# Kernel optimization log

Hardware: AMD Instinct MI355X
Metric: run time of the kernel (lower is better)

## Reference

```python
import jax, jax.numpy as jnp
import numpy as np

K = 3; PAD = 1; STRIDE = 1; EPS = 1e-5


def setup_inputs() -> dict:
    key = jax.random.key(0)
    k0, k1, k2 = jax.random.split(key, 3)
    B, C, H, W, O = 4, 256, 64, 64, 256
    x = jax.random.normal(k0, (B, C, H, W), jnp.float32)
    # offset conv: small random weights so offsets are nontrivial but bounded
    w_off = jax.random.normal(k1, (2 * K * K, C, K, K), jnp.float32) * 0.01
    b_off = jnp.zeros((2 * K * K,), jnp.float32)
    # kaiming normal, mode=fan_out: std = sqrt(2 / (O*K*K))
    w_def = jax.random.normal(k2, (O, C, K, K), jnp.float32) * np.float32(np.sqrt(2.0 / (O * K * K)))
    gamma = jnp.ones((O,), jnp.float32)
    beta = jnp.zeros((O,), jnp.float32)
    return {"x": x, "w_off": w_off, "b_off": b_off, "w_def": w_def, "gamma": gamma, "beta": beta}


def _bilinear_gather(x, py, px):
    """x: [B,C,H,W]; py,px: [B,K2,Ho,Wo] float sample coords.
    Returns [B,K2,Ho,Wo,C] with zero padding outside (per-corner masking,
    matching torchvision deform_conv2d)."""
    B, C, H, W = x.shape
    y0f = jnp.floor(py); x0f = jnp.floor(px)
    wy1 = py - y0f; wy0 = 1.0 - wy1
    wx1 = px - x0f; wx0 = 1.0 - wx1
    bidx = jnp.arange(B)[:, None, None, None]

    def corner(yf, xf, wgt):
        valid = (yf >= 0) & (yf <= H - 1) & (xf >= 0) & (xf <= W - 1)
        yc = jnp.clip(yf.astype(jnp.int32), 0, H - 1)
        xc = jnp.clip(xf.astype(jnp.int32), 0, W - 1)
        v = x[bidx, :, yc, xc]  # [B,K2,Ho,Wo,C] (advanced idx moves C last)
        return v * (wgt * valid)[..., None]

    return (corner(y0f, x0f, wy0 * wx0) + corner(y0f, x0f + 1.0, wy0 * wx1)
            + corner(y0f + 1.0, x0f, wy1 * wx0) + corner(y0f + 1.0, x0f + 1.0, wy1 * wx1))


def _forward(x, w_off, b_off, w_def, gamma, beta):
    B, C, H, W = x.shape
    O = w_def.shape[0]
    K2 = K * K
    # 1) offset-predicting conv
    off = jax.lax.conv_general_dilated(x, w_off, (STRIDE, STRIDE), ((PAD, PAD), (PAD, PAD)))
    off = off + b_off[None, :, None, None]
    Ho, Wo = off.shape[2], off.shape[3]
    off = off.reshape(B, K2, 2, Ho, Wo)  # pairs (dy, dx) per kernel tap
    # 2) deformable sampling locations
    ky, kx = jnp.meshgrid(jnp.arange(K, dtype=jnp.float32), jnp.arange(K, dtype=jnp.float32), indexing='ij')
    base_y = (jnp.arange(Ho, dtype=jnp.float32) * STRIDE - PAD)
    base_x = (jnp.arange(Wo, dtype=jnp.float32) * STRIDE - PAD)
    py = off[:, :, 0] + ky.reshape(K2)[None, :, None, None] + base_y[None, None, :, None]
    px = off[:, :, 1] + kx.reshape(K2)[None, :, None, None] + base_x[None, None, None, :]
    vals = _bilinear_gather(x, py, px)  # [B,K2,Ho,Wo,C]
    # 3) deform conv GEMM (bias=False)
    out = jnp.einsum('bkhwc,ock->bohw', vals, w_def.reshape(O, C, K2))
    # 4) BatchNorm (training mode: batch stats) + ReLU
    mean = out.mean(axis=(0, 2, 3))
    var = out.var(axis=(0, 2, 3))
    out = (out - mean[None, :, None, None]) * (gamma * jax.lax.rsqrt(var + EPS))[None, :, None, None]
    out = out + beta[None, :, None, None]
    return jax.nn.relu(out)


def reference(x, w_off, b_off, w_def, gamma, beta):
    return _forward(x, w_off, b_off, w_def, gamma, beta)
```

## Files before the change

kernel.cpp:

```cpp
#include <hip/hip_runtime.h>
#include <hip/hip_bf16.h>

typedef unsigned int  uint;
typedef unsigned short ushort;
typedef short bf16x8 __attribute__((ext_vector_type(8)));
typedef float f32x4  __attribute__((ext_vector_type(4)));

#define HW   4096
#define KD   2304

__device__ __forceinline__ void load_lds16(const void* g, void* l) {
    __builtin_amdgcn_global_load_lds((const __attribute__((address_space(1))) void*)g,
                                     (__attribute__((address_space(3))) void*)l, 16, 0, 0);
}
__device__ __forceinline__ float blo(uint u) { return __uint_as_float(u << 16); }
__device__ __forceinline__ float bhi(uint u) { return __uint_as_float(u & 0xffff0000u); }
__device__ __forceinline__ uint pack2(float e, float o) {
    __hip_bfloat16 he = __float2bfloat16(e), ho = __float2bfloat16(o);
    return (uint)(*(ushort*)&he) | ((uint)(*(ushort*)&ho) << 16);
}

__global__ void prep_x2(const float* __restrict__ x, uint* __restrict__ x2) {
    int idx = blockIdx.x * 256 + threadIdx.x;
    int a  = idx & 4095;
    int cp = (idx >> 12) & 127;
    int b  = idx >> 19;
    const float* p = x + ((size_t)(b * 256 + 2 * cp)) * HW + a;
    x2[idx] = pack2(p[0], p[HW]);
}

__global__ void prep_bt(const float* __restrict__ w_def, ushort* __restrict__ bt) {
    int idx = blockIdx.x * 256 + threadIdx.x;
    int c   = idx & 255;
    int tap = (idx >> 8) % 9;
    int o   = idx / KD;
    __hip_bfloat16 h = __float2bfloat16(w_def[(o * 256 + c) * 9 + tap]);
    bt[idx] = *(ushort*)&h;
}

__global__ void prep_bt0(const float* __restrict__ w_off, ushort* __restrict__ bt0) {
    int idx = blockIdx.x * 256 + threadIdx.x;
    int c   = idx & 255;
    int tap = (idx >> 8) % 9;
    int j   = idx / KD;
    float v = (j < 18) ? w_off[(j * 256 + c) * 9 + tap] : 0.f;
    __hip_bfloat16 h = __float2bfloat16(v);
    bt0[idx] = *(ushort*)&h;
}

__global__ __launch_bounds__(512) void gemm_off(const uint* __restrict__ x2,
                                                const ushort* __restrict__ bt0,
                                                const float* __restrict__ b_off,
                                                float* __restrict__ off) {
    int id = blockIdx.x;
    int xcd = id & 7;
    int b = xcd >> 1, h = (xcd & 1) * 32 + (id >> 3);
    int t = threadIdx.x, wv = t >> 6, lane = t & 63;
    int mrow = lane & 15, quad = lane >> 4;
    int mq = wv & 3, nn = wv >> 2;

    __shared__ uint   lX[3 * 32 * 64];
    __shared__ ushort lB[32 * 576];

    f32x4 acc = {0.f, 0.f, 0.f, 0.f};

    for (int cb = 0; cb < 4; ++cb) {
#pragma unroll
        for (int s = 0; s < 3; ++s) {
            int q  = s * 8 + wv;
            int dy = q >> 3;
            int y  = h + dy - 1;
            int dl = (q & 7) * 256 + lane * 4;
            int cp = dl >> 6, w4 = dl & 63;
            uint* dst = &lX[q * 256 + lane * 4];
            if ((unsigned)y < 64u) {
                const uint* src = x2 + ((size_t)(b * 128 + cb * 32 + cp)) * HW + y * 64 + w4;
                load_lds16(src, &lX[q * 256]);
            } else {
                uint4 z = {0u, 0u, 0u, 0u};
                *(uint4*)dst = z;
            }
        }
#pragma unroll
        for (int s = 0; s < 5; ++s) {
            int q = s * 8 + wv;
            if (q < 36) {
                int e = q * 512 + lane * 8;
                int o  = e / 576;
                int r  = e - o * 576;
                int chp = r >> 3;
                int ch  = chp ^ (o & 7);
                int tap = ch >> 3, k8 = ch & 7;
                const ushort* src = bt0 + (size_t)o * KD + tap * 256 + cb * 64 + k8 * 8;
                load_lds16(src, &lB[q * 512]);
            }
        }
        __syncthreads();

#pragma unroll
        for (int tap = 0; tap < 9; ++tap) {
            int dy = tap / 3, dx = tap % 3;
            int xx = mq * 16 + mrow + dx - 1;
            bool vx = (unsigned)xx < 64u;
#pragma unroll
            for (int kb = 0; kb < 2; ++kb) {
                int cp0 = kb * 16 + quad * 4;
                uint ad[4];
#pragma unroll
                for (int i = 0; i < 4; ++i)
                    ad[i] = vx ? lX[(dy * 32 + cp0 + i) * 64 + xx] : 0u;
                bf16x8 af = *(bf16x8*)ad;
                int o = nn * 16 + mrow;
                int chs = (tap * 8 + (((kb * 4 + quad)) ^ (o & 7)));
                bf16x8 bfr = *(const bf16x8*)&lB[o * 576 + chs * 8];
                acc = __builtin_amdgcn_mfma_f32_16x16x32_bf16(af, bfr, acc, 0, 0, 0);
            }
        }
        __syncthreads();
    }
    {
        int o = nn * 16 + mrow;
        float bias = (o < 18) ? b_off[o] : 0.f;
        f32x4 v = acc;
        v.x += bias; v.y += bias; v.z += bias; v.w += bias;
        int wpos = mq * 16 + quad * 4;
        *(f32x4*)(off + ((size_t)(b * 32 + o)) * HW + h * 64 + wpos) = v;
    }
}

__global__ __launch_bounds__(1024, 4) void fused_main(const uint* __restrict__ x2,
                                                      const ushort* __restrict__ bt,
                                                      const float* __restrict__ off,
                                                      float* __restrict__ out,
                                                      float* __restrict__ stats) {
    int id = blockIdx.x;
    int xcd = id & 7;
    int b = xcd >> 1, h = (xcd & 1) * 32 + (id >> 3);
    int t = threadIdx.x;
    int wv = t >> 6, lane = t & 63;
    int mrow = lane & 15, quad = lane >> 4;
    bool producer = (wv < 8);
    int w  = t & 63;
    int cq = (t >> 6) & 7;

    __shared__ int    sAc[4][9][64];
    __shared__ float  sWc[4][9][64];
    __shared__ ushort lA[2][64 * 64];
    __shared__ ushort lB[2][256 * 64];

    for (int i = t; i < 576; i += 1024) {
        int tap = i >> 6, ww = i & 63;
        int hw = h * 64 + ww;
        float oy = off[((size_t)(b * 32 + 2 * tap)) * HW + hw];
        float ox = off[((size_t)(b * 32 + 2 * tap + 1)) * HW + hw];
        float py = oy + (float)(tap / 3 + h - 1);
        float px = ox + (float)(tap % 3 + ww - 1);
        float y0f = floorf(py), x0f = floorf(px);
        float wy1 = py - y0f, wx1 = px - x0f;
        float wy0 = 1.f - wy1, wx0 = 1.f - wx1;
        bool vy0 = (y0f >= 0.f) && (y0f <= 63.f);
        bool vy1 = (y0f >= -1.f) && (y0f <= 62.f);
        bool vx0 = (x0f >= 0.f) && (x0f <= 63.f);
        bool vx1 = (x0f >= -1.f) && (x0f <= 62.f);
        int iy0 = min(max((int)y0f, 0), 63),  iy1 = min(max((int)y0f + 1, 0), 63);
        int ix0 = min(max((int)x0f, 0), 63),  ix1 = min(max((int)x0f + 1, 0), 63);
        sAc[0][tap][ww] = iy0 * 64 + ix0;
        sAc[1][tap][ww] = iy0 * 64 + ix1;
        sAc[2][tap][ww] = iy1 * 64 + ix0;
        sAc[3][tap][ww] = iy1 * 64 + ix1;
        sWc[0][tap][ww] = wy0 * wx0 * (float)(vy0 && vx0);
        sWc[1][tap][ww] = wy0 * wx1 * (float)(vy0 && vx1);
        sWc[2][tap][ww] = wy1 * wx0 * (float)(vy1 && vx0);
        sWc[3][tap][ww] = wy1 * wx1 * (float)(vy1 && vx1);
    }
    __syncthreads();

    f32x4 acc[4][2];
#pragma unroll
    for (int m = 0; m < 4; ++m)
#pragma unroll
        for (int n = 0; n < 2; ++n) acc[m][n] = {0.f, 0.f, 0.f, 0.f};

    const uint* xb = x2 + (size_t)(b * 128) * HW;

    auto stage = [&](int sl, ushort* lAb, ushort* lBb) {
        int tap = sl >> 2, cb = sl & 3;
        int a0 = sAc[0][tap][w], a1 = sAc[1][tap][w], a2 = sAc[2][tap][w], a3 = sAc[3][tap][w];
        float f0 = sWc[0][tap][w], f1 = sWc[1][tap][w], f2 = sWc[2][tap][w], f3 = sWc[3][tap][w];
        const uint* xp = xb + (size_t)(cb * 32 + cq * 4) * HW;
        uint u0[4], u1[4], u2[4], u3[4];
#pragma unroll
        for (int j = 0; j < 4; ++j) {
            const uint* pq = xp + (size_t)j * HW;
            u0[j] = pq[a0]; u1[j] = pq[a1]; u2[j] = pq[a2]; u3[j] = pq[a3];
        }
#pragma unroll
        for (int s2 = 0; s2 < 4; ++s2) {
            int e = s2 * 512 + t;
            int o = e >> 3, pp = e & 7;
            int k8 = pp ^ (o & 7);
            const ushort* src = bt + (size_t)o * KD + tap * 256 + cb * 64 + k8 * 8;
            load_lds16(src, &lBb[(e & ~63) * 8]);
        }
        uint r[4];
#pragma unroll
        for (int j = 0; j < 4; ++j) {
            float ev = f0 * blo(u0[j]) + f1 * blo(u1[j]) + f2 * blo(u2[j]) + f3 * blo(u3[j]);
            float ov = f0 * bhi(u0[j]) + f1 * bhi(u1[j]) + f2 * bhi(u2[j]) + f3 * bhi(u3[j]);
            r[j] = pack2(ev, ov);
        }
        uint4 g = {r[0], r[1], r[2], r[3]};
        *(uint4*)&lAb[w * 64 + ((cq ^ (w & 7)) * 8)] = g;
    };

    if (producer) stage(0, lA[0], lB[0]);

    int p = 0;
    for (int s = 0; s < 36; ++s) {
        __syncthreads();
        if (producer) {
            if (s + 1 < 36) stage(s + 1, lA[p ^ 1], lB[p ^ 1]);
        } else {
            int wvc = wv - 8;
#pragma unroll
            for (int kb = 0; kb < 2; ++kb) {
                bf16x8 af[4];
#pragma unroll
                for (int m = 0; m < 4; ++m) {
                    int r = m * 16 + mrow;
                    af[m] = *(const bf16x8*)&lA[p][r * 64 + (((kb * 4 + quad) ^ (r & 7)) * 8)];
                }
#pragma unroll
                for (int n = 0; n < 2; ++n) {
                    int r = wvc * 32 + n * 16 + mrow;
                    bf16x8 bfr = *(const bf16x8*)&lB[p][r * 64 + (((kb * 4 + quad) ^ (r & 7)) * 8)];
#pragma unroll
                    for (int m = 0; m < 4; ++m)
                        acc[m][n] = __builtin_amdgcn_mfma_f32_16x16x32_bf16(af[m], bfr, acc[m][n], 0, 0, 0);
                }
            }
        }
        p ^= 1;
    }

    if (!producer) {
        int wvc = wv - 8;
#pragma unroll
        for (int n = 0; n < 2; ++n) {
            int o = wvc * 32 + n * 16 + mrow;
            float ss = 0.f, qq = 0.f;
#pragma unroll
            for (int m = 0; m < 4; ++m) {
                int pos = m * 16 + quad * 4;
                f32x4 v = acc[m][n];
                *(f32x4*)(out + ((size_t)(b * 256 + o)) * HW + h * 64 + pos) = v;
                ss += v.x + v.y + v.z + v.w;
                qq += v.x * v.x + v.y * v.y + v.z * v.z + v.w * v.w;
            }
            ss += __shfl_xor(ss, 16); ss += __shfl_xor(ss, 32);
            qq += __shfl_xor(qq, 16); qq += __shfl_xor(qq, 32);
            if (quad == 0) {
                atomicAdd(&stats[o], ss);
                atomicAdd(&stats[512 + o], qq);
            }
        }
    }
}

__global__ void bn_finalize(const float* __restrict__ stats,
                            const float* __restrict__ gamma,
                            float* __restrict__ ms) {
    int o = threadIdx.x;
    float S = stats[o], S2 = stats[512 + o];
    float m  = S / 16384.f;
    float var = S2 / 16384.f - m * m;
    ms[o]       = m;
    ms[256 + o] = gamma[o] * rsqrtf(var + 1e-5f);
}

__global__ void bn_apply(float* __restrict__ out,
                         const float* __restrict__ ms,
                         const float* __restrict__ beta) {
    int idx4 = blockIdx.x * 256 + threadIdx.x;
    int o = (idx4 >> 10) & 255;
    float4 v = ((const float4*)out)[idx4];
    float mu = ms[o], sc = ms[256 + o], be = beta[o];
    v.x = fmaxf((v.x - mu) * sc + be, 0.f);
    v.y = fmaxf((v.y - mu) * sc + be, 0.f);
    v.z = fmaxf((v.z - mu) * sc + be, 0.f);
    v.w = fmaxf((v.w - mu) * sc + be, 0.f);
    ((float4*)out)[idx4] = v;
}

extern "C" void kernel_launch(void* const* d_in, const int* in_sizes, int n_in,
                              void* d_out, int out_size, void* d_ws, size_t ws_size,
                              hipStream_t stream) {
    const float* x     = (const float*)d_in[0];
    const float* w_off = (const float*)d_in[1];
    const float* b_off = (const float*)d_in[2];
    const float* w_def = (const float*)d_in[3];
    const float* gamma = (const float*)d_in[4];
    const float* beta  = (const float*)d_in[5];
    float* out = (float*)d_out;

    char* ws = (char*)d_ws;
    uint*   x2    = (uint*)ws;
    ushort* bt    = (ushort*)(ws + 8388608);
    ushort* bt0   = (ushort*)(ws + 9568256);
    float*  off   = (float*)(ws + 9715712);
    float*  stats = (float*)(ws + 11812864);
    float*  ms    = (float*)(ws + 11816960);

    hipMemsetAsync(stats, 0, 4096, stream);
    prep_x2 <<<8192, 256, 0, stream>>>(x, x2);
    prep_bt <<<2304, 256, 0, stream>>>(w_def, bt);
    prep_bt0<<<288,  256, 0, stream>>>(w_off, bt0);
    gemm_off<<<256, 512, 0, stream>>>(x2, bt0, b_off, off);
    fused_main<<<256, 1024, 0, stream>>>(x2, bt, off, out, stats);
    bn_finalize<<<1, 256, 0, stream>>>(stats, gamma, ms);
    bn_apply<<<4096, 256, 0, stream>>>(out, ms, beta);
}
```

Baseline: 179.9 us.

## Store bf16 input channel-innermost (NHWC) for vectorized deformable gathers

The packed bf16 copy of x is now written in a pixel-major, channel-innermost layout through an LDS transpose in the prep kernel. The deformable sampling stage can then fetch four channel pairs per corner with one 16-byte load instead of four scattered 4-byte loads. The offset conv's LDS tile is reorganised to match, with an XOR swizzle so its A fragments become single 16-byte LDS reads. The cost is a more involved transpose in prep and new swizzled indexing that must stay correct.

```diff
diff --git a/kernel.cpp b/kernel.cpp
--- a/kernel.cpp
+++ b/kernel.cpp
@@ -20,13 +20,27 @@
     return (uint)(*(ushort*)&he) | ((uint)(*(ushort*)&ho) << 16);
 }
 
-__global__ void prep_x2(const float* __restrict__ x, uint* __restrict__ x2) {
-    int idx = blockIdx.x * 256 + threadIdx.x;
-    int a  = idx & 4095;
-    int cp = (idx >> 12) & 127;
-    int b  = idx >> 19;
-    const float* p = x + ((size_t)(b * 256 + 2 * cp)) * HW + a;
-    x2[idx] = pack2(p[0], p[HW]);
+__global__ void prep_x2t(const float* __restrict__ x, uint* __restrict__ x2t) {
+    __shared__ uint tl[32][65];
+    int bidx = blockIdx.x;
+    int ab  = bidx & 63;
+    int cpb = (bidx >> 6) & 3;
+    int b   = bidx >> 8;
+    int t = threadIdx.x;
+#pragma unroll
+    for (int i = 0; i < 8; ++i) {
+        int idx = i * 256 + t;
+        int cp = idx >> 6, a = idx & 63;
+        const float* p = x + ((size_t)(b * 256 + (cpb * 32 + cp) * 2)) * HW + ab * 64 + a;
+        tl[cp][a] = pack2(p[0], p[HW]);
+    }
+    __syncthreads();
+#pragma unroll
+    for (int i = 0; i < 8; ++i) {
+        int idx = i * 256 + t;
+        int a = idx >> 5, cp = idx & 31;
+        x2t[((size_t)b * 4096 + ab * 64 + a) * 128 + cpb * 32 + cp] = tl[cp][a];
+    }
 }
 
 __global__ void prep_bt(const float* __restrict__ w_def, ushort* __restrict__ bt) {
@@ -48,7 +62,7 @@
     bt0[idx] = *(ushort*)&h;
 }
 
-__global__ __launch_bounds__(512) void gemm_off(const uint* __restrict__ x2,
+__global__ __launch_bounds__(512) void gemm_off(const uint* __restrict__ x2t,
                                                 const ushort* __restrict__ bt0,
                                                 const float* __restrict__ b_off,
                                                 float* __restrict__ off) {
@@ -59,7 +73,7 @@
     int mrow = lane & 15, quad = lane >> 4;
     int mq = wv & 3, nn = wv >> 2;
 
-    __shared__ uint   lX[3 * 32 * 64];
+    __shared__ uint   lX[3 * 64 * 32];
     __shared__ ushort lB[32 * 576];
 
     f32x4 acc = {0.f, 0.f, 0.f, 0.f};
@@ -67,18 +81,18 @@
     for (int cb = 0; cb < 4; ++cb) {
 #pragma unroll
         for (int s = 0; s < 3; ++s) {
-            int q  = s * 8 + wv;
-            int dy = q >> 3;
-            int y  = h + dy - 1;
-            int dl = (q & 7) * 256 + lane * 4;
-            int cp = dl >> 6, w4 = dl & 63;
-            uint* dst = &lX[q * 256 + lane * 4];
+            int q   = s * 8 + wv;
+            int dy  = q >> 3;
+            int y   = h + dy - 1;
+            int sub = q & 7;
+            int wl  = sub * 8 + (lane >> 3);
+            int cps = ((lane & 7) ^ ((lane >> 3) & 7)) * 4;
             if ((unsigned)y < 64u) {
-                const uint* src = x2 + ((size_t)(b * 128 + cb * 32 + cp)) * HW + y * 64 + w4;
+                const uint* src = x2t + ((size_t)(b * 4096 + y * 64 + wl)) * 128 + cb * 32 + cps;
                 load_lds16(src, &lX[q * 256]);
             } else {
                 uint4 z = {0u, 0u, 0u, 0u};
-                *(uint4*)dst = z;
+                *(uint4*)&lX[q * 256 + lane * 4] = z;
             }
         }
 #pragma unroll
@@ -102,14 +116,13 @@
             int dy = tap / 3, dx = tap % 3;
             int xx = mq * 16 + mrow + dx - 1;
             bool vx = (unsigned)xx < 64u;
+            int xc = min(max(xx, 0), 63);
 #pragma unroll
             for (int kb = 0; kb < 2; ++kb) {
                 int cp0 = kb * 16 + quad * 4;
-                uint ad[4];
-#pragma unroll
-                for (int i = 0; i < 4; ++i)
-                    ad[i] = vx ? lX[(dy * 32 + cp0 + i) * 64 + xx] : 0u;
-                bf16x8 af = *(bf16x8*)ad;
+                uint4 ad = {0u, 0u, 0u, 0u};
+                if (vx) ad = *(const uint4*)&lX[dy * 2048 + xc * 32 + (cp0 ^ ((xc & 7) * 4))];
+                bf16x8 af = *(bf16x8*)&ad;
                 int o = nn * 16 + mrow;
                 int chs = (tap * 8 + (((kb * 4 + quad)) ^ (o & 7)));
                 bf16x8 bfr = *(const bf16x8*)&lB[o * 576 + chs * 8];
@@ -128,7 +141,7 @@
     }
 }
 
-__global__ __launch_bounds__(1024, 4) void fused_main(const uint* __restrict__ x2,
+__global__ __launch_bounds__(1024, 4) void fused_main(const uint* __restrict__ x2t,
                                                       const ushort* __restrict__ bt,
                                                       const float* __restrict__ off,
                                                       float* __restrict__ out,
@@ -181,19 +194,17 @@
 #pragma unroll
         for (int n = 0; n < 2; ++n) acc[m][n] = {0.f, 0.f, 0.f, 0.f};
 
-    const uint* xb = x2 + (size_t)(b * 128) * HW;
+    const uint* xb = x2t + (size_t)b * 4096 * 128;
 
     auto stage = [&](int sl, ushort* lAb, ushort* lBb) {
         int tap = sl >> 2, cb = sl & 3;
         int a0 = sAc[0][tap][w], a1 = sAc[1][tap][w], a2 = sAc[2][tap][w], a3 = sAc[3][tap][w];
         float f0 = sWc[0][tap][w], f1 = sWc[1][tap][w], f2 = sWc[2][tap][w], f3 = sWc[3][tap][w];
-        const uint* xp = xb + (size_t)(cb * 32 + cq * 4) * HW;
-        uint u0[4], u1[4], u2[4], u3[4];
-#pragma unroll
-        for (int j = 0; j < 4; ++j) {
-            const uint* pq = xp + (size_t)j * HW;
-            u0[j] = pq[a0]; u1[j] = pq[a1]; u2[j] = pq[a2]; u3[j] = pq[a3];
-        }
+        const uint* xp = xb + cb * 32 + cq * 4;
+        uint4 v0 = *(const uint4*)(xp + (size_t)a0 * 128);
+        uint4 v1 = *(const uint4*)(xp + (size_t)a1 * 128);
+        uint4 v2 = *(const uint4*)(xp + (size_t)a2 * 128);
+        uint4 v3 = *(const uint4*)(xp + (size_t)a3 * 128);
 #pragma unroll
         for (int s2 = 0; s2 < 4; ++s2) {
             int e = s2 * 512 + t;
@@ -202,11 +213,15 @@
             const ushort* src = bt + (size_t)o * KD + tap * 256 + cb * 64 + k8 * 8;
             load_lds16(src, &lBb[(e & ~63) * 8]);
         }
+        const uint* c0 = (const uint*)&v0;
+        const uint* c1 = (const uint*)&v1;
+        const uint* c2 = (const uint*)&v2;
+        const uint* c3 = (const uint*)&v3;
         uint r[4];
 #pragma unroll
         for (int j = 0; j < 4; ++j) {
-            float ev = f0 * blo(u0[j]) + f1 * blo(u1[j]) + f2 * blo(u2[j]) + f3 * blo(u3[j]);
-            float ov = f0 * bhi(u0[j]) + f1 * bhi(u1[j]) + f2 * bhi(u2[j]) + f3 * bhi(u3[j]);
+            float ev = f0 * blo(c0[j]) + f1 * blo(c1[j]) + f2 * blo(c2[j]) + f3 * blo(c3[j]);
+            float ov = f0 * bhi(c0[j]) + f1 * bhi(c1[j]) + f2 * bhi(c2[j]) + f3 * bhi(c3[j]);
             r[j] = pack2(ev, ov);
         }
         uint4 g = {r[0], r[1], r[2], r[3]};
@@ -304,7 +319,7 @@
     float* out = (float*)d_out;
 
     char* ws = (char*)d_ws;
-    uint*   x2    = (uint*)ws;
+    uint*   x2t   = (uint*)ws;
     ushort* bt    = (ushort*)(ws + 8388608);
     ushort* bt0   = (ushort*)(ws + 9568256);
     float*  off   = (float*)(ws + 9715712);
@@ -312,11 +327,11 @@
     float*  ms    = (float*)(ws + 11816960);
 
     hipMemsetAsync(stats, 0, 4096, stream);
-    prep_x2 <<<8192, 256, 0, stream>>>(x, x2);
+    prep_x2t<<<1024, 256, 0, stream>>>(x, x2t);
     prep_bt <<<2304, 256, 0, stream>>>(w_def, bt);
     prep_bt0<<<288,  256, 0, stream>>>(w_off, bt0);
-    gemm_off<<<256, 512, 0, stream>>>(x2, bt0, b_off, off);
-    fused_main<<<256, 1024, 0, stream>>>(x2, bt, off, out, stats);
+    gemm_off<<<256, 512, 0, stream>>>(x2t, bt0, b_off, off);
+    fused_main<<<256, 1024, 0, stream>>>(x2t, bt, off, out, stats);
     bn_finalize<<<1, 256, 0, stream>>>(stats, gamma, ms);
     bn_apply<<<4096, 256, 0, stream>>>(out, ms, beta);
 }
```

Result: faster. 165.9 us (-7.8%).
